# Performance work log

Measured on AMD Instinct MI355X. Metric: run time of the kernel, lower is better.

The kernel has to match this reference:

```python
import jax, jax.numpy as jnp
import numpy as np

VOCAB, EMB, UNITS, B, T = 32000, 256, 1024, 64, 128


def setup_inputs() -> dict:
    key = jax.random.key(0)
    ks = jax.random.split(key, 16)
    s = lambda fan_in: 1.0 / np.sqrt(fan_in)
    inp = {
        "x": jax.random.randint(ks[0], (B, 1), 0, VOCAB),
        "hidden": jax.random.normal(ks[1], (B, UNITS), dtype=jnp.float32),
        "enc_output": jax.random.normal(ks[2], (B, T, UNITS), dtype=jnp.float32),
        "emb": jax.random.normal(ks[3], (VOCAB, EMB), dtype=jnp.float32) * 0.02,
        "W1": jax.random.normal(ks[4], (UNITS, UNITS), dtype=jnp.float32) * s(UNITS),
        "b1": jnp.zeros((UNITS,), jnp.float32),
        "W2": jax.random.normal(ks[5], (UNITS, UNITS), dtype=jnp.float32) * s(UNITS),
        "b2": jnp.zeros((UNITS,), jnp.float32),
        "V": jax.random.normal(ks[6], (UNITS, 1), dtype=jnp.float32) * s(UNITS),
        "bV": jnp.zeros((1,), jnp.float32),
        "gru_k": jax.random.normal(ks[7], (UNITS + EMB, 3 * UNITS), dtype=jnp.float32) * s(UNITS + EMB),
        "gru_rk": jax.random.normal(ks[8], (UNITS, 3 * UNITS), dtype=jnp.float32) * s(UNITS),
        "gru_b": jnp.zeros((3 * UNITS,), jnp.float32),
        "fc_W": jax.random.normal(ks[9], (UNITS, VOCAB), dtype=jnp.float32) * s(UNITS),
        "fc_b": jnp.zeros((VOCAB,), jnp.float32),
    }
    return inp


def reference(x, hidden, enc_output, emb, W1, b1, W2, b2, V, bV,
              gru_k, gru_rk, gru_b, fc_W, fc_b):
    # Bahdanau additive attention over encoder steps
    # score: [B, T, 1]
    score = jnp.tanh(enc_output @ W1 + b1 + (hidden @ W2 + b2)[:, None, :]) @ V + bV
    attention_weights = jax.nn.softmax(score, axis=1)              # [B, T, 1]
    context = jnp.sum(attention_weights * enc_output, axis=1)      # [B, UNITS]

    xe = emb[x[:, 0]]                                              # [B, EMB]
    gin = jnp.concatenate([context, xe], axis=-1)                  # [B, UNITS+EMB]

    # Single GRU step; original calls gru(x) with no initial_state -> h0 = 0
    h0 = jnp.zeros((x.shape[0], gru_rk.shape[0]), gin.dtype)
    u = x.shape[1]  # unused; seq len is 1
    gates_x = gin @ gru_k + gru_b                                  # [B, 3*UNITS]
    gates_h = h0 @ gru_rk                                          # [B, 3*UNITS]
    n = gru_rk.shape[0]
    z = jax.nn.sigmoid(gates_x[:, :n] + gates_h[:, :n])
    r = jax.nn.sigmoid(gates_x[:, n:2 * n] + gates_h[:, n:2 * n])
    hh = jnp.tanh(gates_x[:, 2 * n:] + r * gates_h[:, 2 * n:])
    state = z * h0 + (1.0 - z) * hh                                # [B, UNITS]

    logits = state @ fc_W + fc_b                                   # [B, VOCAB]
    return logits, state, attention_weights
```

## Files before the change

kernel.cpp:

```cpp
#include <hip/hip_runtime.h>
#include <math.h>

#define UNITS 1024
#define EMBD  256
#define BATCH 64
#define TLEN  128
#define VOCAB 32000
#define GIN_D (UNITS + EMBD)

typedef short short8 __attribute__((ext_vector_type(8)));
typedef float f32x4  __attribute__((ext_vector_type(4)));

__device__ __forceinline__ unsigned short f2bf(float f) {
    unsigned int u = __float_as_uint(f);
    u += 0x7fffu + ((u >> 16) & 1u);
    return (unsigned short)(u >> 16);
}
__device__ __forceinline__ unsigned int packbf(float lo, float hi) {
    return (unsigned int)f2bf(lo) | ((unsigned int)f2bf(hi) << 16);
}

__global__ __launch_bounds__(256) void k_c(const float* __restrict__ hidden,
                                           const float* __restrict__ W2,
                                           const float* __restrict__ b1,
                                           const float* __restrict__ b2,
                                           float* __restrict__ c) {
    const int lane = threadIdx.x & 63;
    const int j = blockIdx.x * 64 + lane;
    const int b = blockIdx.y * 4 + (threadIdx.x >> 6);
    const int k0 = blockIdx.z * 256;
    const float* hrow = hidden + (size_t)b * UNITS + k0;
    const float* wcol = W2 + (size_t)k0 * UNITS + j;
    float acc = 0.f;
#pragma unroll 8
    for (int k = 0; k < 256; ++k)
        acc = fmaf(hrow[k], wcol[(size_t)k * UNITS], acc);
    if (blockIdx.z == 0) acc += b1[j] + b2[j];
    atomicAdd(&c[(size_t)b * UNITS + j], acc);
}

__global__ __launch_bounds__(256, 2) void k_score(const float* __restrict__ enc,
                                                  const float* __restrict__ W1,
                                                  const float* __restrict__ c,
                                                  const float* __restrict__ V,
                                                  float* __restrict__ score) {
    __shared__ unsigned short As[128 * 72];
    __shared__ unsigned short Bs[128 * 72];
    const int jt   = blockIdx.x;
    const int b    = blockIdx.y;
    const int tid  = threadIdx.x;
    const int lane = tid & 63;
    const int wid  = tid >> 6;
    const int wr   = wid & 1;
    const int wc   = wid >> 1;
    const int quad = lane >> 4;
    const int l16  = lane & 15;

    const float* encb = enc + (size_t)b * TLEN * UNITS;
    const float* w1b  = W1 + jt * 128;

    f32x4 acc[4][4];
#pragma unroll
    for (int i = 0; i < 4; ++i)
#pragma unroll
        for (int j = 0; j < 4; ++j)
            acc[i][j] = (f32x4){0.f, 0.f, 0.f, 0.f};

    const int ar = tid >> 4;
    const int ac = tid & 15;
    const int bp = tid >> 5;
    const int bj = tid & 31;

    for (int kc = 0; kc < UNITS; kc += 64) {
        float4 av[8];
#pragma unroll
        for (int rr = 0; rr < 8; ++rr)
            av[rr] = *(const float4*)(encb + (size_t)(ar + rr * 16) * UNITS + kc + ac * 4);
        float4 bv0[4], bv1[4];
#pragma unroll
        for (int kk = 0; kk < 4; ++kk) {
            const int k0 = 2 * (bp + 8 * kk);
            bv0[kk] = *(const float4*)(w1b + (size_t)(kc + k0) * UNITS + bj * 4);
            bv1[kk] = *(const float4*)(w1b + (size_t)(kc + k0 + 1) * UNITS + bj * 4);
        }
        __syncthreads();
#pragma unroll
        for (int rr = 0; rr < 8; ++rr) {
            ushort4 h;
            h.x = f2bf(av[rr].x); h.y = f2bf(av[rr].y);
            h.z = f2bf(av[rr].z); h.w = f2bf(av[rr].w);
            *(ushort4*)&As[(ar + rr * 16) * 72 + ac * 4] = h;
        }
#pragma unroll
        for (int kk = 0; kk < 4; ++kk) {
            const int k0 = 2 * (bp + 8 * kk);
            *(unsigned int*)&Bs[(bj * 4 + 0) * 72 + k0] = packbf(bv0[kk].x, bv1[kk].x);
            *(unsigned int*)&Bs[(bj * 4 + 1) * 72 + k0] = packbf(bv0[kk].y, bv1[kk].y);
            *(unsigned int*)&Bs[(bj * 4 + 2) * 72 + k0] = packbf(bv0[kk].z, bv1[kk].z);
            *(unsigned int*)&Bs[(bj * 4 + 3) * 72 + k0] = packbf(bv0[kk].w, bv1[kk].w);
        }
        __syncthreads();
#pragma unroll
        for (int kk = 0; kk < 2; ++kk) {
            const int kb = kk * 32 + quad * 8;
            short8 af[4], bfr[4];
#pragma unroll
            for (int mt = 0; mt < 4; ++mt)
                af[mt] = *(const short8*)&As[(wr * 64 + mt * 16 + l16) * 72 + kb];
#pragma unroll
            for (int nt = 0; nt < 4; ++nt)
                bfr[nt] = *(const short8*)&Bs[(wc * 64 + nt * 16 + l16) * 72 + kb];
#pragma unroll
            for (int mt = 0; mt < 4; ++mt)
#pragma unroll
                for (int nt = 0; nt < 4; ++nt)
                    acc[mt][nt] = __builtin_amdgcn_mfma_f32_16x16x32_bf16(
                        af[mt], bfr[nt], acc[mt][nt], 0, 0, 0);
        }
    }

    float cv[4], vv[4];
#pragma unroll
    for (int nt = 0; nt < 4; ++nt) {
        const int col = wc * 64 + nt * 16 + l16;
        cv[nt] = c[(size_t)b * UNITS + jt * 128 + col];
        vv[nt] = V[jt * 128 + col];
    }
    float rs[16];
#pragma unroll
    for (int mt = 0; mt < 4; ++mt)
#pragma unroll
        for (int reg = 0; reg < 4; ++reg) {
            float s = 0.f;
#pragma unroll
            for (int nt = 0; nt < 4; ++nt)
                s += tanhf(acc[mt][nt][reg] + cv[nt]) * vv[nt];
            rs[mt * 4 + reg] = s;
        }
#pragma unroll
    for (int off = 1; off < 16; off <<= 1)
#pragma unroll
        for (int i = 0; i < 16; ++i)
            rs[i] += __shfl_xor(rs[i], off);
    if (l16 == 0) {
#pragma unroll
        for (int mt = 0; mt < 4; ++mt)
#pragma unroll
            for (int reg = 0; reg < 4; ++reg)
                atomicAdd(&score[b * TLEN + wr * 64 + mt * 16 + quad * 4 + reg],
                          rs[mt * 4 + reg]);
    }
}

__global__ void k_softmax(const float* __restrict__ score, float* __restrict__ attw) {
    const int b = blockIdx.x;
    const int lane = threadIdx.x;
    float s0 = score[b * TLEN + lane];
    float s1 = score[b * TLEN + 64 + lane];
    float m = fmaxf(s0, s1);
#pragma unroll
    for (int off = 1; off < 64; off <<= 1) m = fmaxf(m, __shfl_xor(m, off));
    const float e0 = expf(s0 - m);
    const float e1 = expf(s1 - m);
    float s = e0 + e1;
#pragma unroll
    for (int off = 1; off < 64; off <<= 1) s += __shfl_xor(s, off);
    const float inv = 1.f / s;
    attw[b * TLEN + lane] = e0 * inv;
    attw[b * TLEN + 64 + lane] = e1 * inv;
}

__global__ __launch_bounds__(256) void k_context(const float* __restrict__ enc,
                                                 const float* __restrict__ attw,
                                                 float* __restrict__ gin) {
    const int b = blockIdx.y;
    const int k = blockIdx.x * 256 + threadIdx.x;
    __shared__ float w[TLEN];
    if (threadIdx.x < TLEN) w[threadIdx.x] = attw[b * TLEN + threadIdx.x];
    __syncthreads();
    const float* e = enc + (size_t)b * TLEN * UNITS + k;
    float acc = 0.f;
#pragma unroll 8
    for (int t = 0; t < TLEN; ++t)
        acc = fmaf(w[t], e[(size_t)t * UNITS], acc);
    gin[(size_t)b * GIN_D + k] = acc;
}

__global__ void k_embed(const int* __restrict__ x, const float* __restrict__ emb,
                        float* __restrict__ gin) {
    const int b = blockIdx.x;
    const int e = threadIdx.x;
    const int row = x[b];
    gin[(size_t)b * GIN_D + UNITS + e] = emb[(size_t)row * EMBD + e];
}

__global__ __launch_bounds__(256) void k_gru_acc(const float* __restrict__ gin,
                                                 const float* __restrict__ gru_k,
                                                 const float* __restrict__ gru_b,
                                                 float* __restrict__ gz,
                                                 float* __restrict__ gh) {
    const int lane = threadIdx.x & 63;
    const int i = blockIdx.x * 64 + lane;
    const int b = blockIdx.y * 4 + (threadIdx.x >> 6);
    const int k0 = blockIdx.z * 256;
    const float* g = gin + (size_t)b * GIN_D + k0;
    const float* wz = gru_k + (size_t)k0 * 3072 + i;
    const float* wh = wz + 2048;
    float az = 0.f, ah = 0.f;
#pragma unroll 8
    for (int k = 0; k < 256; ++k) {
        const float gv = g[k];
        az = fmaf(gv, wz[(size_t)k * 3072], az);
        ah = fmaf(gv, wh[(size_t)k * 3072], ah);
    }
    if (blockIdx.z == 0) { az += gru_b[i]; ah += gru_b[2048 + i]; }
    atomicAdd(&gz[(size_t)b * UNITS + i], az);
    atomicAdd(&gh[(size_t)b * UNITS + i], ah);
}

__global__ __launch_bounds__(256) void k_gru_fin(const float* __restrict__ gz,
                                                 const float* __restrict__ gh,
                                                 float* __restrict__ state,
                                                 float* __restrict__ stateT) {
    const int lane = threadIdx.x & 63;
    const int i = blockIdx.x * 64 + lane;
    const int b = blockIdx.y * 4 + (threadIdx.x >> 6);
    const float az = gz[(size_t)b * UNITS + i];
    const float ah = gh[(size_t)b * UNITS + i];
    const float z = 1.f / (1.f + expf(-az));
    const float hh = tanhf(ah);
    const float st = (1.f - z) * hh;
    state[(size_t)b * UNITS + i] = st;
    stateT[(size_t)i * BATCH + b] = st;
}

__global__ __launch_bounds__(256, 2) void k_fc(const float* __restrict__ stateT,
                                               const float* __restrict__ fc_W,
                                               const float* __restrict__ fc_b,
                                               float* __restrict__ logits) {
    __shared__ float sState[1024 * 16];
    const int tid  = threadIdx.x;
    const int lane = tid & 63;
    const int wid  = tid >> 6;
    const int g0   = blockIdx.y * 16;
    const int col0 = blockIdx.x * 256 + lane * 4;

#pragma unroll
    for (int it = 0; it < 16; ++it) {
        const int idx = tid + it * 256;
        const int r = idx >> 2, cch = idx & 3;
        const float4 v = *(const float4*)(stateT + (size_t)r * BATCH + g0 + cch * 4);
        *(float4*)&sState[r * 16 + cch * 4] = v;
    }

    const int krow0 = wid * 256;
    const float* wbase = fc_W + col0;

    float4 wr[4];
#pragma unroll
    for (int j = 0; j < 4; ++j)
        wr[j] = *(const float4*)(wbase + (size_t)(krow0 + j) * VOCAB);

    __syncthreads();

    float4 acc[16];
#pragma unroll
    for (int b = 0; b < 16; ++b) acc[b] = (float4){0.f, 0.f, 0.f, 0.f};

    float4 srng[2][4];
#pragma unroll
    for (int c = 0; c < 4; ++c)
        srng[0][c] = *(const float4*)&sState[krow0 * 16 + c * 4];

#define FC_SUBSTEP(J, PREFETCH_W, PREFETCH_S)                                  \
    {                                                                          \
        const int r = krow0 + k + (J);                                         \
        if (PREFETCH_S) {                                                      \
            _Pragma("unroll")                                                  \
            for (int c = 0; c < 4; ++c)                                        \
                srng[((J) + 1) & 1][c] = *(const float4*)&sState[(r + 1) * 16 + c * 4]; \
        }                                                                      \
        const float4 wv = wr[(J)];                                             \
        if (PREFETCH_W)                                                        \
            wr[(J)] = *(const float4*)(wbase + (size_t)(r + 4) * VOCAB);       \
        _Pragma("unroll")                                                      \
        for (int c = 0; c < 4; ++c) {                                          \
            const float4 sv = srng[(J) & 1][c];                                \
            acc[c * 4 + 0].x = fmaf(wv.x, sv.x, acc[c * 4 + 0].x);             \
            acc[c * 4 + 0].y = fmaf(wv.y, sv.x, acc[c * 4 + 0].y);             \
            acc[c * 4 + 0].z = fmaf(wv.z, sv.x, acc[c * 4 + 0].z);             \
            acc[c * 4 + 0].w = fmaf(wv.w, sv.x, acc[c * 4 + 0].w);             \
            acc[c * 4 + 1].x = fmaf(wv.x, sv.y, acc[c * 4 + 1].x);             \
            acc[c * 4 + 1].y = fmaf(wv.y, sv.y, acc[c * 4 + 1].y);             \
            acc[c * 4 + 1].z = fmaf(wv.z, sv.y, acc[c * 4 + 1].z);             \
            acc[c * 4 + 1].w = fmaf(wv.w, sv.y, acc[c * 4 + 1].w);             \
            acc[c * 4 + 2].x = fmaf(wv.x, sv.z, acc[c * 4 + 2].x);             \
            acc[c * 4 + 2].y = fmaf(wv.y, sv.z, acc[c * 4 + 2].y);             \
            acc[c * 4 + 2].z = fmaf(wv.z, sv.z, acc[c * 4 + 2].z);             \
            acc[c * 4 + 2].w = fmaf(wv.w, sv.z, acc[c * 4 + 2].w);             \
            acc[c * 4 + 3].x = fmaf(wv.x, sv.w, acc[c * 4 + 3].x);             \
            acc[c * 4 + 3].y = fmaf(wv.y, sv.w, acc[c * 4 + 3].y);             \
            acc[c * 4 + 3].z = fmaf(wv.z, sv.w, acc[c * 4 + 3].z);             \
            acc[c * 4 + 3].w = fmaf(wv.w, sv.w, acc[c * 4 + 3].w);             \
        }                                                                      \
    }

    for (int k = 0; k < 252; k += 4) {
        FC_SUBSTEP(0, true, true)
        FC_SUBSTEP(1, true, true)
        FC_SUBSTEP(2, true, true)
        FC_SUBSTEP(3, true, true)
    }
    {
        const int k = 252;
        FC_SUBSTEP(0, false, true)
        FC_SUBSTEP(1, false, true)
        FC_SUBSTEP(2, false, true)
        FC_SUBSTEP(3, false, false)
    }
#undef FC_SUBSTEP

    __syncthreads();
    float* rbuf = sState;
#pragma unroll 1
    for (int ph = 0; ph < 4; ++ph) {
        if (wid == ph) {
#pragma unroll
            for (int b = 0; b < 16; ++b) {
                float4* p = (float4*)&rbuf[b * 256 + lane * 4];
                if (ph == 0) {
                    *p = acc[b];
                } else {
                    float4 t = *p;
                    t.x += acc[b].x; t.y += acc[b].y;
                    t.z += acc[b].z; t.w += acc[b].w;
                    *p = t;
                }
            }
        }
        __syncthreads();
    }

    const int bb = tid >> 4;
    const int ch = tid & 15;
    const int cbase = blockIdx.x * 256 + ch * 16;
    float* lp = logits + (size_t)(g0 + bb) * VOCAB + cbase;
#pragma unroll
    for (int q = 0; q < 4; ++q) {
        float4 t = *(float4*)&rbuf[bb * 256 + ch * 16 + q * 4];
        const float4 fb = *(const float4*)(fc_b + cbase + q * 4);
        t.x += fb.x; t.y += fb.y; t.z += fb.z; t.w += fb.w;
        *(float4*)(lp + q * 4) = t;
    }
}

extern "C" void kernel_launch(void* const* d_in, const int* in_sizes, int n_in,
                              void* d_out, int out_size, void* d_ws, size_t ws_size,
                              hipStream_t stream) {
    const int*   x      = (const int*)  d_in[0];
    const float* hidden = (const float*)d_in[1];
    const float* enc    = (const float*)d_in[2];
    const float* emb    = (const float*)d_in[3];
    const float* W1     = (const float*)d_in[4];
    const float* b1     = (const float*)d_in[5];
    const float* W2     = (const float*)d_in[6];
    const float* b2     = (const float*)d_in[7];
    const float* V      = (const float*)d_in[8];
    const float* gru_k  = (const float*)d_in[10];
    const float* gru_b  = (const float*)d_in[12];
    const float* fc_W   = (const float*)d_in[13];
    const float* fc_b   = (const float*)d_in[14];

    float* out       = (float*)d_out;
    float* logits    = out;
    float* state_out = out + (size_t)BATCH * VOCAB;
    float* attw      = state_out + (size_t)BATCH * UNITS;

    float* c      = (float*)d_ws;
    float* score  = c + 65536;
    float* gin    = score + 8192;
    float* stateT = gin + 81920;
    float* gz     = stateT + 65536;
    float* gh     = gz + 65536;

    hipMemsetAsync(c, 0, (size_t)BATCH * UNITS * sizeof(float), stream);
    hipMemsetAsync(score, 0, (size_t)BATCH * TLEN * sizeof(float), stream);
    hipMemsetAsync(gz, 0, (size_t)2 * BATCH * UNITS * sizeof(float), stream);

    k_c      <<<dim3(16, 16, 4), 256, 0, stream>>>(hidden, W2, b1, b2, c);
    k_score  <<<dim3(8, 64),     256, 0, stream>>>(enc, W1, c, V, score);
    k_softmax<<<64, 64, 0, stream>>>(score, attw);
    k_context<<<dim3(4, 64),     256, 0, stream>>>(enc, attw, gin);
    k_embed  <<<64, 256, 0, stream>>>(x, emb, gin);
    k_gru_acc<<<dim3(16, 16, 5), 256, 0, stream>>>(gin, gru_k, gru_b, gz, gh);
    k_gru_fin<<<dim3(16, 16),    256, 0, stream>>>(gz, gh, state_out, stateT);
    k_fc     <<<dim3(125, 4),    256, 0, stream>>>(stateT, fc_W, fc_b, logits);
}
```

Before: 453.0 us.

## Pre-transpose W1 to bf16 and split score tiles across batch halves

A new kernel transposes W1 into a bf16 [j][k] layout once per call, so k_score can load B tiles as contiguous 16-byte chunks without per-element conversion or strided LDS stores. k_score now uses 64x128 tiles with a grid of 128x8 blocks and 4 blocks per CU, doubling block count for occupancy. The cost is an extra kernel launch plus a read of W1 and a write of 2MB, and W1 is now reread per batch half.

```diff
diff --git a/kernel.cpp b/kernel.cpp
--- a/kernel.cpp
+++ b/kernel.cpp
@@ -16,8 +16,26 @@
     u += 0x7fffu + ((u >> 16) & 1u);
     return (unsigned short)(u >> 16);
 }
-__device__ __forceinline__ unsigned int packbf(float lo, float hi) {
-    return (unsigned int)f2bf(lo) | ((unsigned int)f2bf(hi) << 16);
+
+__global__ __launch_bounds__(256) void k_w1t(const float* __restrict__ W1,
+                                             unsigned short* __restrict__ w1t) {
+    __shared__ float t[64][65];
+    const int tid = threadIdx.x;
+    const int bx = blockIdx.x * 64;
+    const int by = blockIdx.y * 64;
+#pragma unroll
+    for (int p = 0; p < 16; ++p) {
+        const int idx = tid + p * 256;
+        const int r = idx >> 6, cc = idx & 63;
+        t[r][cc] = W1[(size_t)(bx + r) * UNITS + by + cc];
+    }
+    __syncthreads();
+#pragma unroll
+    for (int p = 0; p < 16; ++p) {
+        const int idx = tid + p * 256;
+        const int jr = idx >> 6, kc = idx & 63;
+        w1t[(size_t)(by + jr) * UNITS + bx + kc] = f2bf(t[kc][jr]);
+    }
 }
 
 __global__ __launch_bounds__(256) void k_c(const float* __restrict__ hidden,
@@ -39,92 +57,87 @@
     atomicAdd(&c[(size_t)b * UNITS + j], acc);
 }
 
-__global__ __launch_bounds__(256, 2) void k_score(const float* __restrict__ enc,
-                                                  const float* __restrict__ W1,
+__global__ __launch_bounds__(256, 4) void k_score(const float* __restrict__ enc,
+                                                  const unsigned short* __restrict__ w1t,
                                                   const float* __restrict__ c,
                                                   const float* __restrict__ V,
                                                   float* __restrict__ score) {
-    __shared__ unsigned short As[128 * 72];
+    __shared__ unsigned short As[64 * 72];
     __shared__ unsigned short Bs[128 * 72];
-    const int jt   = blockIdx.x;
-    const int b    = blockIdx.y;
+    const int half = blockIdx.x & 1;
+    const int b    = blockIdx.x >> 1;
+    const int jt   = blockIdx.y;
     const int tid  = threadIdx.x;
     const int lane = tid & 63;
-    const int wid  = tid >> 6;
-    const int wr   = wid & 1;
-    const int wc   = wid >> 1;
+    const int wc   = tid >> 6;
     const int quad = lane >> 4;
     const int l16  = lane & 15;
 
-    const float* encb = enc + (size_t)b * TLEN * UNITS;
-    const float* w1b  = W1 + jt * 128;
-
-    f32x4 acc[4][4];
+    const float* encb = enc + (size_t)b * TLEN * UNITS + (size_t)half * 64 * UNITS;
+    const unsigned short* w1b = w1t + (size_t)jt * 128 * UNITS;
+
+    f32x4 acc[4][2];
 #pragma unroll
     for (int i = 0; i < 4; ++i)
 #pragma unroll
-        for (int j = 0; j < 4; ++j)
+        for (int j = 0; j < 2; ++j)
             acc[i][j] = (f32x4){0.f, 0.f, 0.f, 0.f};
 
     const int ar = tid >> 4;
     const int ac = tid & 15;
-    const int bp = tid >> 5;
-    const int bj = tid & 31;
 
     for (int kc = 0; kc < UNITS; kc += 64) {
-        float4 av[8];
-#pragma unroll
-        for (int rr = 0; rr < 8; ++rr)
+        float4 av[4];
+#pragma unroll
+        for (int rr = 0; rr < 4; ++rr)
             av[rr] = *(const float4*)(encb + (size_t)(ar + rr * 16) * UNITS + kc + ac * 4);
-        float4 bv0[4], bv1[4];
-#pragma unroll
-        for (int kk = 0; kk < 4; ++kk) {
-            const int k0 = 2 * (bp + 8 * kk);
-            bv0[kk] = *(const float4*)(w1b + (size_t)(kc + k0) * UNITS + bj * 4);
-            bv1[kk] = *(const float4*)(w1b + (size_t)(kc + k0 + 1) * UNITS + bj * 4);
+        short8 bv[4];
+#pragma unroll
+        for (int p = 0; p < 4; ++p) {
+            const int cidx = tid + p * 256;
+            const int row = cidx >> 3, ch = cidx & 7;
+            bv[p] = *(const short8*)(w1b + (size_t)row * UNITS + kc + ch * 8);
         }
         __syncthreads();
 #pragma unroll
-        for (int rr = 0; rr < 8; ++rr) {
+        for (int rr = 0; rr < 4; ++rr) {
             ushort4 h;
             h.x = f2bf(av[rr].x); h.y = f2bf(av[rr].y);
             h.z = f2bf(av[rr].z); h.w = f2bf(av[rr].w);
             *(ushort4*)&As[(ar + rr * 16) * 72 + ac * 4] = h;
         }
 #pragma unroll
-        for (int kk = 0; kk < 4; ++kk) {
-            const int k0 = 2 * (bp + 8 * kk);
-            *(unsigned int*)&Bs[(bj * 4 + 0) * 72 + k0] = packbf(bv0[kk].x, bv1[kk].x);
-            *(unsigned int*)&Bs[(bj * 4 + 1) * 72 + k0] = packbf(bv0[kk].y, bv1[kk].y);
-            *(unsigned int*)&Bs[(bj * 4 + 2) * 72 + k0] = packbf(bv0[kk].z, bv1[kk].z);
-            *(unsigned int*)&Bs[(bj * 4 + 3) * 72 + k0] = packbf(bv0[kk].w, bv1[kk].w);
+        for (int p = 0; p < 4; ++p) {
+            const int cidx = tid + p * 256;
+            const int row = cidx >> 3, ch = cidx & 7;
+            *(short8*)&Bs[row * 72 + ch * 8] = bv[p];
         }
         __syncthreads();
 #pragma unroll
         for (int kk = 0; kk < 2; ++kk) {
             const int kb = kk * 32 + quad * 8;
-            short8 af[4], bfr[4];
+            short8 af[4], bfr[2];
 #pragma unroll
             for (int mt = 0; mt < 4; ++mt)
-                af[mt] = *(const short8*)&As[(wr * 64 + mt * 16 + l16) * 72 + kb];
-#pragma unroll
-            for (int nt = 0; nt < 4; ++nt)
-                bfr[nt] = *(const short8*)&Bs[(wc * 64 + nt * 16 + l16) * 72 + kb];
+                af[mt] = *(const short8*)&As[(mt * 16 + l16) * 72 + kb];
+#pragma unroll
+            for (int nt = 0; nt < 2; ++nt)
+                bfr[nt] = *(const short8*)&Bs[(wc * 32 + nt * 16 + l16) * 72 + kb];
 #pragma unroll
             for (int mt = 0; mt < 4; ++mt)
 #pragma unroll
-                for (int nt = 0; nt < 4; ++nt)
+                for (int nt = 0; nt < 2; ++nt)
                     acc[mt][nt] = __builtin_amdgcn_mfma_f32_16x16x32_bf16(
                         af[mt], bfr[nt], acc[mt][nt], 0, 0, 0);
         }
     }
 
-    float cv[4], vv[4];
-#pragma unroll
-    for (int nt = 0; nt < 4; ++nt) {
-        const int col = wc * 64 + nt * 16 + l16;
-        cv[nt] = c[(size_t)b * UNITS + jt * 128 + col];
-        vv[nt] = V[jt * 128 + col];
+    float cv[2], vv[2];
+#pragma unroll
+    for (int nt = 0; nt < 2; ++nt) {
+        const int col = jt * 128 + wc * 32 + nt * 16 + l16;
+        cv[nt] = c[(size_t)b * UNITS + col];
+        vv[nt] = V[col];
     }
     float rs[16];
 #pragma unroll
@@ -133,7 +146,7 @@
         for (int reg = 0; reg < 4; ++reg) {
             float s = 0.f;
 #pragma unroll
-            for (int nt = 0; nt < 4; ++nt)
+            for (int nt = 0; nt < 2; ++nt)
                 s += tanhf(acc[mt][nt][reg] + cv[nt]) * vv[nt];
             rs[mt * 4 + reg] = s;
         }
@@ -147,7 +160,7 @@
         for (int mt = 0; mt < 4; ++mt)
 #pragma unroll
             for (int reg = 0; reg < 4; ++reg)
-                atomicAdd(&score[b * TLEN + wr * 64 + mt * 16 + quad * 4 + reg],
+                atomicAdd(&score[b * TLEN + half * 64 + mt * 16 + quad * 4 + reg],
                           rs[mt * 4 + reg]);
     }
 }
@@ -382,13 +395,15 @@
     float* stateT = gin + 81920;
     float* gz     = stateT + 65536;
     float* gh     = gz + 65536;
+    unsigned short* w1t = (unsigned short*)(gh + 65536);
 
     hipMemsetAsync(c, 0, (size_t)BATCH * UNITS * sizeof(float), stream);
     hipMemsetAsync(score, 0, (size_t)BATCH * TLEN * sizeof(float), stream);
     hipMemsetAsync(gz, 0, (size_t)2 * BATCH * UNITS * sizeof(float), stream);
 
+    k_w1t    <<<dim3(16, 16),    256, 0, stream>>>(W1, w1t);
     k_c      <<<dim3(16, 16, 4), 256, 0, stream>>>(hidden, W2, b1, b2, c);
-    k_score  <<<dim3(8, 64),     256, 0, stream>>>(enc, W1, c, V, score);
+    k_score  <<<dim3(128, 8),    256, 0, stream>>>(enc, w1t, c, V, score);
     k_softmax<<<64, 64, 0, stream>>>(score, attw);
     k_context<<<dim3(4, 64),     256, 0, stream>>>(enc, attw, gin);
     k_embed  <<<64, 256, 0, stream>>>(x, emb, gin);
```

New measurement: 408.9 us. 1.11x faster.
